# Kernel tuning notes

Hardware: AMD Instinct MI355X
Metric: run time of the kernel (lower is better)

The kernel has to match this reference:

```python
import jax, jax.numpy as jnp
import numpy as np

THRESHOLD = 33.33  # torch forward default

def setup_inputs() -> dict:
    key = jax.random.key(0)
    k1, k2 = jax.random.split(key)
    source_pc = jax.random.normal(k1, (2, 16384, 3), dtype=jnp.float32)
    target_pc = jax.random.normal(k2, (2, 16384, 3), dtype=jnp.float32)
    return {"source_pc": source_pc, "target_pc": target_pc}

def _pairwise_dist(x, y):
    # Euclidean cdist via the matmul expansion (same math as torch.cdist p=2).
    # x: [B, N, D], y: [B, M, D] -> [B, N, M]
    x2 = jnp.sum(x * x, axis=-1)              # [B, N]
    y2 = jnp.sum(y * y, axis=-1)              # [B, M]
    xy = jnp.einsum('bnd,bmd->bnm', x, y)     # [B, N, M]
    d2 = x2[:, :, None] + y2[None if False else slice(None), None, :] - 2.0 * xy
    d2 = x2[:, :, None] + y2[:, None, :] - 2.0 * xy
    return jnp.sqrt(jnp.maximum(d2, 0.0))

def reference(source_pc, target_pc):
    dist = _pairwise_dist(source_pc.astype(jnp.float32), target_pc.astype(jnp.float32))
    dist1 = jnp.minimum(jnp.min(dist, axis=2), THRESHOLD)  # [B, N] clamped
    dist2 = jnp.minimum(jnp.min(dist, axis=1), THRESHOLD)  # [B, M] clamped
    d1 = jnp.mean(dist1, axis=-1)
    d2 = jnp.mean(dist2, axis=-1)
    return (d1 + d2) / 2.0  # bidirectional=True default -> [B]
```

## Files before the change

kernel.cpp:

```cpp
#include <hip/hip_runtime.h>

#define NPTS 16384
#define TH 33.33f

typedef __attribute__((ext_vector_type(8)))  __bf16 bf16x8;
typedef __attribute__((ext_vector_type(16))) float  f32x16;

__device__ __forceinline__ unsigned short f2bf(float x) {
    unsigned u = __float_as_uint(x);
    u += 0x7FFFu + ((u >> 16) & 1u);
    return (unsigned short)(u >> 16);
}
__device__ __forceinline__ float bf2f(unsigned short h) {
    return __uint_as_float(((unsigned)h) << 16);
}

union UV { uint4 v; bf16x8 h; unsigned short s[8]; };


#define FOLD2(MM, AA) { \
    f32x16 t0 = __builtin_amdgcn_mfma_f32_32x32x16_bf16(AA, q0, zc, 0, 0, 0); \
    f32x16 t1 = __builtin_amdgcn_mfma_f32_32x32x16_bf16(AA, q1, zc, 0, 0, 0); \
    _Pragma("unroll") for (int j = 0; j < 16; j++) MM[j] = fmaxf(fmaxf(t0[j], t1[j]), MM[j]); }

__device__ __forceinline__ void conv_store(unsigned short* lb, int k,
                                           float x, float y, float z) {
    float hp = 0.5f * fmaf(z, z, fmaf(y, y, x * x));
    unsigned short xh = f2bf(x), yh = f2bf(y), zh = f2bf(z);
    unsigned short xl = f2bf(x - bf2f(xh)), yl = f2bf(y - bf2f(yh)), zl = f2bf(z - bf2f(zh));
    float rr = hp;
    unsigned short h0 = f2bf(rr); rr -= bf2f(h0);
    unsigned short h1 = f2bf(rr); rr -= bf2f(h1);
    unsigned short h2 = f2bf(rr);
    UV c0, c1;
    c0.s[0]=xh; c0.s[1]=yh; c0.s[2]=zh; c0.s[3]=xh; c0.s[4]=yh; c0.s[5]=zh; c0.s[6]=xl; c0.s[7]=yl;
    c1.s[0]=zl; c1.s[1]=(unsigned short)(h0^0x8000); c1.s[2]=(unsigned short)(h1^0x8000);
    c1.s[3]=(unsigned short)(h2^0x8000); c1.s[4]=0; c1.s[5]=0; c1.s[6]=0; c1.s[7]=0;
    int t = k >> 5, pos = k & 31;
    *(uint4*)(lb + t * 512 + pos * 8)       = c0.v;
    *(uint4*)(lb + t * 512 + 256 + pos * 8) = c1.v;
}

#define LOAD_PTS(CC) { \
    const float* g0 = pp + (size_t)(seg * 2048 + (CC) * 512 + tid) * 3; \
    px0 = g0[0]; py0 = g0[1]; pz0 = g0[2]; \
    const float* g1 = g0 + 768; \
    px1 = g1[0]; py1 = g1[1]; pz1 = g1[2]; }

#define CONV_WRITE(BUF) { \
    unsigned short* lb = (unsigned short*)(smem + (BUF) * 16384); \
    conv_store(lb, tid,       px0, py0, pz0); \
    conv_store(lb, tid + 256, px1, py1, pz1); }

#define EPILOG(MM, P) { \
    float* sc = scratch + wave * 1056; \
    _Pragma("unroll") for (int j = 0; j < 16; j++) { \
        int r0 = (j & 3) + 8 * (j >> 2) + 4 * g; sc[r0 * 33 + cc] = MM[j]; } \
    __syncthreads(); \
    const float* sr = sc + cc * 33 + g * 16; \
    float mx = -3.0e38f; \
    _Pragma("unroll") for (int k = 0; k < 16; k++) mx = fmaxf(mx, sr[k]); \
    mx = fmaxf(mx, __shfl_xor(mx, 32, 64)); \
    if (lane < 32) { \
        float d2 = 2.0f * (hq[P] - mx); \
        float d = fminf(sqrtf(fmaxf(d2, 0.0f)), TH); \
        dst[wave * 64 + (P) * 32 + lane] = d; } \
    __syncthreads(); }

__global__ __launch_bounds__(256, 4) void chamfer_kernel(
        const float* __restrict__ src, const float* __restrict__ tgt,
        float* __restrict__ d2part, float* __restrict__ out)
{
    const int db = blockIdx.y, dir = db >> 1, b = db & 1;
    const int rowblock = blockIdx.x >> 3, seg = blockIdx.x & 7;
    const int tid = threadIdx.x, wave = tid >> 6, lane = tid & 63;
    const int g = lane >> 5, cc = lane & 31;
    if (blockIdx.x == 0 && db == 0 && tid < 2) out[tid] = 0.0f;
    const float* qp = (dir == 0 ? src : tgt) + (size_t)b * NPTS * 3;
    const float* pp = (dir == 0 ? tgt : src) + (size_t)b * NPTS * 3;
    const unsigned short one = 0x3F80;

    __shared__ alignas(16) unsigned char smem[32768];
    float* scratch = (float*)smem;

    const int rt0 = rowblock * 8 + wave * 2;
    bf16x8 afrag[2]; float hq[2];
#pragma unroll
    for (int i = 0; i < 2; i++) {
        int r = (rt0 + i) * 32 + cc;
        float x = qp[r * 3 + 0], y = qp[r * 3 + 1], z = qp[r * 3 + 2];
        hq[i] = 0.5f * fmaf(z, z, fmaf(y, y, x * x));
        unsigned short xh = f2bf(x), yh = f2bf(y), zh = f2bf(z);
        unsigned short xl = f2bf(x - bf2f(xh)), yl = f2bf(y - bf2f(yh)), zl = f2bf(z - bf2f(zh));
        UV f0, f1, rv;
        f0.s[0]=xh; f0.s[1]=yh; f0.s[2]=zh; f0.s[3]=xl; f0.s[4]=yl; f0.s[5]=zl; f0.s[6]=xh; f0.s[7]=yh;
        f1.s[0]=zh; f1.s[1]=one; f1.s[2]=one; f1.s[3]=one; f1.s[4]=0; f1.s[5]=0; f1.s[6]=0; f1.s[7]=0;
        rv.v = g ? f1.v : f0.v;
        afrag[i] = rv.h;
    }

    f32x16 m0 = -3.0e38f, m1 = -3.0e38f;
    const f32x16 zc = 0.0f;
    float px0, py0, pz0, px1, py1, pz1;

    LOAD_PTS(0)
    CONV_WRITE(0)
    __syncthreads();
#pragma unroll 1
    for (int c = 0; c < 4; ++c) {
        if (c < 3) LOAD_PTS(c + 1)
        const unsigned short* bb = (const unsigned short*)(smem + (c & 1) * 16384);
#pragma unroll 1
        for (int pt = 0; pt < 8; ++pt) {
            bf16x8 q0 = *(const bf16x8*)(bb + pt * 1024 + lane * 8);
            bf16x8 q1 = *(const bf16x8*)(bb + pt * 1024 + 512 + lane * 8);
            FOLD2(m0, afrag[0])
            FOLD2(m1, afrag[1])
        }
        if (c < 3) CONV_WRITE((c + 1) & 1)
        __syncthreads();
    }

    float* dst = d2part + (((size_t)(db * 64 + rowblock)) * 8 + seg) * 256;
    EPILOG(m0, 0)
    EPILOG(m1, 1)
}

__global__ __launch_bounds__(256) void merge_kernel(const float* __restrict__ d2part,
                                                    float* __restrict__ out) {
    const int b = blockIdx.y;
    const int slice = blockIdx.x;
    const int tid = threadIdx.x;
    float s = 0.0f;
#pragma unroll
    for (int pass = 0; pass < 2; pass++) {
        const float* base = d2part + (size_t)(pass * 2 + b) * 64 * 8 * 256;
#pragma unroll
        for (int i = 0; i < 4; i++) {
            int r = slice * 1024 + i * 256 + tid;
            const float* p = base + (size_t)(r >> 8) * 2048 + (r & 255);
            float m = p[0];
#pragma unroll
            for (int sgi = 1; sgi < 8; sgi++) m = fminf(m, p[sgi * 256]);
            s += m;
        }
    }
#pragma unroll
    for (int off = 32; off > 0; off >>= 1) s += __shfl_down(s, off, 64);
    __shared__ float w[4];
    if ((tid & 63) == 0) w[tid >> 6] = s;
    __syncthreads();
    if (tid == 0) {
        float t = (w[0] + w[1]) + (w[2] + w[3]);
        atomicAdd(&out[b], t * (1.0f / (2.0f * NPTS)));
    }
}

extern "C" void kernel_launch(void* const* d_in, const int* in_sizes, int n_in,
                              void* d_out, int out_size, void* d_ws, size_t ws_size,
                              hipStream_t stream) {
    const float* src = (const float*)d_in[0];
    const float* tgt = (const float*)d_in[1];
    float* out = (float*)d_out;
    float* d2part = (float*)d_ws;

    chamfer_kernel<<<dim3(512, 4), 256, 0, stream>>>(src, tgt, d2part, out);
    merge_kernel<<<dim3(16, 2), 256, 0, stream>>>(d2part, out);
}
```

Measured before the change: 91.32 us.

## Compute both chamfer directions from one distance matrix pass with column atomics

Instead of running the MFMA distance sweep twice (source→target and target→source), the kernel folds both squared-norm terms into the bf16 MMA operands so the output is the full negated half-distance. It then reduces the same tiles both row-wise and column-wise, and column maxima go through shared-memory atomicMax and then global atomicMin on sqrt distances. This halves the MFMA work and grid. In exchange it adds per-tile tree reductions, LDS atomics and global atomics, plus a memset launch. The +256 offset trick for ordering float bits assumes the values stay above -256.

```diff
diff --git a/kernel.cpp b/kernel.cpp
--- a/kernel.cpp
+++ b/kernel.cpp
@@ -18,10 +18,23 @@
 union UV { uint4 v; bf16x8 h; unsigned short s[8]; };
 
 
-#define FOLD2(MM, AA) { \
+#define TREE16(R, T) { \
+    float u0 = fmaxf(T[0], T[8]),  u1 = fmaxf(T[1], T[9]); \
+    float u2 = fmaxf(T[2], T[10]), u3 = fmaxf(T[3], T[11]); \
+    float u4 = fmaxf(T[4], T[12]), u5 = fmaxf(T[5], T[13]); \
+    float u6 = fmaxf(T[6], T[14]), u7 = fmaxf(T[7], T[15]); \
+    u0 = fmaxf(u0, u4); u1 = fmaxf(u1, u5); u2 = fmaxf(u2, u6); u3 = fmaxf(u3, u7); \
+    u0 = fmaxf(u0, u2); u1 = fmaxf(u1, u3); \
+    R = fmaxf(u0, u1); }
+
+#define FOLDC(MM, AA, CA, CB) { \
     f32x16 t0 = __builtin_amdgcn_mfma_f32_32x32x16_bf16(AA, q0, zc, 0, 0, 0); \
     f32x16 t1 = __builtin_amdgcn_mfma_f32_32x32x16_bf16(AA, q1, zc, 0, 0, 0); \
-    _Pragma("unroll") for (int j = 0; j < 16; j++) MM[j] = fmaxf(fmaxf(t0[j], t1[j]), MM[j]); }
+    _Pragma("unroll") for (int j = 0; j < 16; j++) MM[j] = fmaxf(fmaxf(t0[j], t1[j]), MM[j]); \
+    float ra, rb; \
+    TREE16(ra, t0) \
+    TREE16(rb, t1) \
+    CA = fmaxf(CA, ra); CB = fmaxf(CB, rb); }
 
 __device__ __forceinline__ void conv_store(unsigned short* lb, int k,
                                            float x, float y, float z) {
@@ -32,10 +45,11 @@
     unsigned short h0 = f2bf(rr); rr -= bf2f(h0);
     unsigned short h1 = f2bf(rr); rr -= bf2f(h1);
     unsigned short h2 = f2bf(rr);
+    const unsigned short one = 0x3F80;
     UV c0, c1;
     c0.s[0]=xh; c0.s[1]=yh; c0.s[2]=zh; c0.s[3]=xh; c0.s[4]=yh; c0.s[5]=zh; c0.s[6]=xl; c0.s[7]=yl;
     c1.s[0]=zl; c1.s[1]=(unsigned short)(h0^0x8000); c1.s[2]=(unsigned short)(h1^0x8000);
-    c1.s[3]=(unsigned short)(h2^0x8000); c1.s[4]=0; c1.s[5]=0; c1.s[6]=0; c1.s[7]=0;
+    c1.s[3]=(unsigned short)(h2^0x8000); c1.s[4]=one; c1.s[5]=one; c1.s[6]=one; c1.s[7]=0;
     int t = k >> 5, pos = k & 31;
     *(uint4*)(lb + t * 512 + pos * 8)       = c0.v;
     *(uint4*)(lb + t * 512 + 256 + pos * 8) = c1.v;
@@ -62,39 +76,47 @@
     _Pragma("unroll") for (int k = 0; k < 16; k++) mx = fmaxf(mx, sr[k]); \
     mx = fmaxf(mx, __shfl_xor(mx, 32, 64)); \
     if (lane < 32) { \
-        float d2 = 2.0f * (hq[P] - mx); \
+        float d2 = -2.0f * mx; \
         float d = fminf(sqrtf(fmaxf(d2, 0.0f)), TH); \
         dst[wave * 64 + (P) * 32 + lane] = d; } \
     __syncthreads(); }
 
 __global__ __launch_bounds__(256, 4) void chamfer_kernel(
         const float* __restrict__ src, const float* __restrict__ tgt,
-        float* __restrict__ d2part, float* __restrict__ out)
+        float* __restrict__ row_part, unsigned int* __restrict__ colmin_g,
+        float* __restrict__ out)
 {
-    const int db = blockIdx.y, dir = db >> 1, b = db & 1;
+    const int b = blockIdx.y;
     const int rowblock = blockIdx.x >> 3, seg = blockIdx.x & 7;
     const int tid = threadIdx.x, wave = tid >> 6, lane = tid & 63;
     const int g = lane >> 5, cc = lane & 31;
-    if (blockIdx.x == 0 && db == 0 && tid < 2) out[tid] = 0.0f;
-    const float* qp = (dir == 0 ? src : tgt) + (size_t)b * NPTS * 3;
-    const float* pp = (dir == 0 ? tgt : src) + (size_t)b * NPTS * 3;
+    if (blockIdx.x == 0 && b == 0 && tid < 2) out[tid] = 0.0f;
+    const float* qp = src + (size_t)b * NPTS * 3;
+    const float* pp = tgt + (size_t)b * NPTS * 3;
     const unsigned short one = 0x3F80;
 
     __shared__ alignas(16) unsigned char smem[32768];
+    __shared__ unsigned int colsmax[512];
     float* scratch = (float*)smem;
 
     const int rt0 = rowblock * 8 + wave * 2;
-    bf16x8 afrag[2]; float hq[2];
+    bf16x8 afrag[2];
 #pragma unroll
     for (int i = 0; i < 2; i++) {
         int r = (rt0 + i) * 32 + cc;
         float x = qp[r * 3 + 0], y = qp[r * 3 + 1], z = qp[r * 3 + 2];
-        hq[i] = 0.5f * fmaf(z, z, fmaf(y, y, x * x));
+        float hq = 0.5f * fmaf(z, z, fmaf(y, y, x * x));
         unsigned short xh = f2bf(x), yh = f2bf(y), zh = f2bf(z);
         unsigned short xl = f2bf(x - bf2f(xh)), yl = f2bf(y - bf2f(yh)), zl = f2bf(z - bf2f(zh));
+        float rr = hq;
+        unsigned short h0 = f2bf(rr); rr -= bf2f(h0);
+        unsigned short h1 = f2bf(rr); rr -= bf2f(h1);
+        unsigned short h2 = f2bf(rr);
         UV f0, f1, rv;
         f0.s[0]=xh; f0.s[1]=yh; f0.s[2]=zh; f0.s[3]=xl; f0.s[4]=yl; f0.s[5]=zl; f0.s[6]=xh; f0.s[7]=yh;
-        f1.s[0]=zh; f1.s[1]=one; f1.s[2]=one; f1.s[3]=one; f1.s[4]=0; f1.s[5]=0; f1.s[6]=0; f1.s[7]=0;
+        f1.s[0]=zh; f1.s[1]=one; f1.s[2]=one; f1.s[3]=one;
+        f1.s[4]=(unsigned short)(h0^0x8000); f1.s[5]=(unsigned short)(h1^0x8000);
+        f1.s[6]=(unsigned short)(h2^0x8000); f1.s[7]=0;
         rv.v = g ? f1.v : f0.v;
         afrag[i] = rv.h;
     }
@@ -103,6 +125,7 @@
     const f32x16 zc = 0.0f;
     float px0, py0, pz0, px1, py1, pz1;
 
+    colsmax[tid] = 0u; colsmax[tid + 256] = 0u;
     LOAD_PTS(0)
     CONV_WRITE(0)
     __syncthreads();
@@ -114,36 +137,48 @@
         for (int pt = 0; pt < 8; ++pt) {
             bf16x8 q0 = *(const bf16x8*)(bb + pt * 1024 + lane * 8);
             bf16x8 q1 = *(const bf16x8*)(bb + pt * 1024 + 512 + lane * 8);
-            FOLD2(m0, afrag[0])
-            FOLD2(m1, afrag[1])
+            float ca = -3.0e38f, cb = -3.0e38f;
+            FOLDC(m0, afrag[0], ca, cb)
+            FOLDC(m1, afrag[1], ca, cb)
+            atomicMax(&colsmax[pt * 64 + cc],      __float_as_uint(ca + 256.0f));
+            atomicMax(&colsmax[pt * 64 + 32 + cc], __float_as_uint(cb + 256.0f));
+        }
+        __syncthreads();
+        {
+            unsigned v0 = colsmax[tid], v1 = colsmax[tid + 256];
+            colsmax[tid] = 0u; colsmax[tid + 256] = 0u;
+            float s0 = __uint_as_float(v0) - 256.0f;
+            float s1 = __uint_as_float(v1) - 256.0f;
+            float dd0 = fminf(sqrtf(fmaxf(-2.0f * s0, 0.0f)), TH);
+            float dd1 = fminf(sqrtf(fmaxf(-2.0f * s1, 0.0f)), TH);
+            unsigned int* gc = colmin_g + (size_t)b * NPTS + seg * 2048 + c * 512;
+            atomicMin(&gc[tid],       __float_as_uint(dd0));
+            atomicMin(&gc[tid + 256], __float_as_uint(dd1));
         }
         if (c < 3) CONV_WRITE((c + 1) & 1)
         __syncthreads();
     }
 
-    float* dst = d2part + (((size_t)(db * 64 + rowblock)) * 8 + seg) * 256;
+    float* dst = row_part + ((size_t)(b * 64 + rowblock) * 8 + seg) * 256;
     EPILOG(m0, 0)
     EPILOG(m1, 1)
 }
 
-__global__ __launch_bounds__(256) void merge_kernel(const float* __restrict__ d2part,
-                                                    float* __restrict__ out) {
+__global__ __launch_bounds__(256) void merge_kernel(const float* __restrict__ row_part,
+        const unsigned int* __restrict__ colmin_g, float* __restrict__ out) {
     const int b = blockIdx.y;
     const int slice = blockIdx.x;
     const int tid = threadIdx.x;
     float s = 0.0f;
 #pragma unroll
-    for (int pass = 0; pass < 2; pass++) {
-        const float* base = d2part + (size_t)(pass * 2 + b) * 64 * 8 * 256;
-#pragma unroll
-        for (int i = 0; i < 4; i++) {
-            int r = slice * 1024 + i * 256 + tid;
-            const float* p = base + (size_t)(r >> 8) * 2048 + (r & 255);
-            float m = p[0];
-#pragma unroll
-            for (int sgi = 1; sgi < 8; sgi++) m = fminf(m, p[sgi * 256]);
-            s += m;
-        }
+    for (int i = 0; i < 4; i++) {
+        int r = slice * 1024 + i * 256 + tid;
+        const float* p = row_part + ((size_t)(b * 64 + (r >> 8)) * 8) * 256 + (r & 255);
+        float m = p[0];
+#pragma unroll
+        for (int sg = 1; sg < 8; sg++) m = fminf(m, p[sg * 256]);
+        s += m;
+        s += __uint_as_float(colmin_g[(size_t)b * NPTS + r]);
     }
 #pragma unroll
     for (int off = 32; off > 0; off >>= 1) s += __shfl_down(s, off, 64);
@@ -162,8 +197,10 @@
     const float* src = (const float*)d_in[0];
     const float* tgt = (const float*)d_in[1];
     float* out = (float*)d_out;
-    float* d2part = (float*)d_ws;
-
-    chamfer_kernel<<<dim3(512, 4), 256, 0, stream>>>(src, tgt, d2part, out);
-    merge_kernel<<<dim3(16, 2), 256, 0, stream>>>(d2part, out);
-}
+    float* row_part = (float*)d_ws;
+    unsigned int* colmin_g = (unsigned int*)((char*)d_ws + 1048576);
+
+    hipMemsetAsync(colmin_g, 0xFF, 2 * NPTS * sizeof(unsigned int), stream);
+    chamfer_kernel<<<dim3(512, 2), 256, 0, stream>>>(src, tgt, row_part, colmin_g, out);
+    merge_kernel<<<dim3(16, 2), 256, 0, stream>>>(row_part, colmin_g, out);
+}
```

Result: slower. 95.26 us (+4.3%).
